# Kernel optimization log

Hardware: AMD Instinct MI355X
Metric: run time of the kernel (lower is better)

The kernel has to match this reference:

```python
import jax, jax.numpy as jnp
import numpy as np

B, L, D, T = 32, 1024, 1024, 10  # batch, seq_len, d_model, num_tags


def setup_inputs() -> dict:
    key = jax.random.key(0)
    ks = jax.random.split(key, 6)
    embeddings = jax.random.normal(ks[0], (B, L, D), jnp.float32)
    attention_mask = jnp.ones((B, L), jnp.int32)  # torchcrf requires mask[:,0]==1
    labels = jax.random.randint(ks[1], (B, L), 0, T)
    conv_w = jax.random.normal(ks[2], (T, D, 3), jnp.float32) * 0.02  # [out,in,k] torch layout
    conv_b = jnp.zeros((T,), jnp.float32)
    start_transitions = jax.random.uniform(ks[3], (T,), jnp.float32, -0.1, 0.1)
    end_transitions = jax.random.uniform(ks[4], (T,), jnp.float32, -0.1, 0.1)
    transitions = jax.random.uniform(ks[5], (T, T), jnp.float32, -0.1, 0.1)
    return dict(embeddings=embeddings, attention_mask=attention_mask, labels=labels,
                conv_w=conv_w, conv_b=conv_b, start_transitions=start_transitions,
                end_transitions=end_transitions, transitions=transitions)


def _crf_nll(emissions, labels, mask_bool, start_transitions, end_transitions, transitions):
    # emissions [B,L,T], labels [B,L] int, mask_bool [B,L]
    b, l, t = emissions.shape
    maskf = mask_bool.astype(emissions.dtype)
    # ---- numerator: score of the given tag path ----
    em_tag = jnp.take_along_axis(emissions, labels[..., None], axis=-1)[..., 0]  # [B,L]
    trans_sc = transitions[labels[:, :-1], labels[:, 1:]]                         # [B,L-1]
    num = start_transitions[labels[:, 0]] + em_tag[:, 0]
    num = num + ((trans_sc + em_tag[:, 1:]) * maskf[:, 1:]).sum(-1)
    seq_len = maskf.sum(-1).astype(jnp.int32)                                     # [B]
    last_tags = labels[jnp.arange(b), seq_len - 1]
    num = num + end_transitions[last_tags]
    # ---- denominator: forward algorithm (log partition), lax.scan over time ----
    alpha0 = start_transitions + emissions[:, 0]                                  # [B,T]

    def step(alpha, xs):
        em_t, m_t = xs  # [B,T], [B]
        nxt = jax.nn.logsumexp(alpha[:, :, None] + transitions[None] + em_t[:, None, :], axis=1)
        return jnp.where(m_t[:, None], nxt, alpha), None

    alpha, _ = jax.lax.scan(step, alpha0,
                            (emissions[:, 1:].transpose(1, 0, 2), mask_bool[:, 1:].T))
    denom = jax.nn.logsumexp(alpha + end_transitions, axis=1)                     # [B]
    return -(num - denom).sum()  # torchcrf reduction='sum', model negates


def reference(embeddings, attention_mask, labels, conv_w, conv_b,
              start_transitions, end_transitions, transitions):
    # Conv1d(d_model -> num_tags, k=3, padding='same') on [B,D,L]
    x = embeddings.transpose(0, 2, 1)  # [B,D,L]
    em = jax.lax.conv_general_dilated(x, conv_w, (1,), 'SAME',
                                      dimension_numbers=('NCH', 'OIH', 'NCH'))
    em = em.transpose(0, 2, 1) + conv_b  # [B,L,T]
    mask_bool = attention_mask.astype(bool)
    return _crf_nll(em, labels, mask_bool, start_transitions, end_transitions, transitions)
```

## Files before the change

### kernel.cpp

```cpp
#include <hip/hip_runtime.h>


#define LNEG -1e30f

static constexpr int B = 32, L = 1024, D = 1024;
static constexpr int CS = 64;
static constexpr int NC = 16;

static constexpr size_t EMPAD_OFF    = 0;
static constexpr size_t CHUNKP_OFF   = (size_t)B * L * 16;
static constexpr size_t CHUNKOFF_OFF = CHUNKP_OFF + (size_t)B * NC * 100;
static constexpr size_t WB_OFF       = CHUNKOFF_OFF + (size_t)B * NC * 12;

typedef __attribute__((ext_vector_type(8))) short short8;
typedef __attribute__((ext_vector_type(4))) short short4v;
typedef __attribute__((ext_vector_type(4))) float v4f;

static __device__ inline short f2bf(float f) {
    unsigned u = __float_as_uint(f);
    unsigned r = (u + 0x7FFFu + ((u >> 16) & 1u)) >> 16;
    return (short)r;
}

__global__ __launch_bounds__(256) void init_kernel(
    const float* __restrict__ w, short* __restrict__ WB, float* __restrict__ out)
{
    const int gid    = blockIdx.x * 256 + threadIdx.x;
    const int stride = gridDim.x * 256;
    for (int i = gid; i < 49152; i += stride) {
        const int k8 = i >> 7;
        const int r  = i & 127;
        const int t  = r >> 3;
        const int j  = r & 7;
        const int k  = (k8 << 3) | j;
        const int kk = k >> 10;
        const int d  = k & 1023;
        WB[i] = (t < 10) ? f2bf(w[t * (D * 3) + d * 3 + kk]) : (short)0;
    }
    if (gid == 0) out[0] = 0.f;
}

static constexpr int SROW = 136;
static constexpr int LDSN = 18 * SROW;

__global__ __launch_bounds__(64) void conv_mfma_kernel(
    const float* __restrict__ emb, const short* __restrict__ WB,
    const float* __restrict__ bias, float* __restrict__ emPad)
{
    __shared__ short lds[2 * LDSN];

    const int lane = threadIdx.x;
    const int b    = blockIdx.x >> 6;
    const int l0   = (blockIdx.x & 63) << 4;
    const int g    = lane >> 4;
    const int m    = lane & 15;

    const float* embB = emb + (size_t)b * (L * D);

    v4f acc0 = {0.f, 0.f, 0.f, 0.f};
    v4f acc1 = {0.f, 0.f, 0.f, 0.f};
    v4f acc2 = {0.f, 0.f, 0.f, 0.f};

    float4 pre[9];

#define PREF(CH) do {                                                         \
    const int d0_ = (CH) * 128;                                               \
    _Pragma("unroll")                                                         \
    for (int it = 0; it < 9; ++it) {                                          \
        const int idx = lane + it * 64;                                       \
        const int r_ = idx >> 5, c4 = idx & 31;                               \
        const int gl = l0 + r_ - 1;                                           \
        float4 v = make_float4(0.f, 0.f, 0.f, 0.f);                           \
        if ((unsigned)gl < (unsigned)L)                                       \
            v = *(const float4*)(embB + (size_t)gl * D + d0_ + c4 * 4);       \
        pre[it] = v;                                                          \
    } } while (0)

#define COMMIT(BUF) do {                                                      \
    short* base_ = lds + (BUF) * LDSN;                                        \
    _Pragma("unroll")                                                         \
    for (int it = 0; it < 9; ++it) {                                          \
        const int idx = lane + it * 64;                                       \
        const int r_ = idx >> 5, c4 = idx & 31;                               \
        short4v s;                                                            \
        s.x = f2bf(pre[it].x); s.y = f2bf(pre[it].y);                         \
        s.z = f2bf(pre[it].z); s.w = f2bf(pre[it].w);                         \
        *(short4v*)(base_ + r_ * SROW + c4 * 4) = s;                          \
    } } while (0)

    PREF(0);
    COMMIT(0);
    __syncthreads();

    for (int dc = 0; dc < 8; ++dc) {
        if (dc < 7) PREF(dc + 1);

        const short* bufp = lds + (dc & 1) * LDSN;
#pragma unroll
        for (int kk = 0; kk < 3; ++kk) {
            const short* arow = bufp + (m + kk) * SROW + g * 8;
            const short* wp   = WB + ((size_t)(kk * 128 + dc * 16 + g)) * 128 + m * 8;
#pragma unroll
            for (int ds = 0; ds < 4; ++ds) {
                const short8 a  = *(const short8*)(arow + ds * 32);
                const short8 bf = *(const short8*)(wp + (size_t)ds * 4 * 128);
                if (kk == 0)      acc0 = __builtin_amdgcn_mfma_f32_16x16x32_bf16(a, bf, acc0, 0, 0, 0);
                else if (kk == 1) acc1 = __builtin_amdgcn_mfma_f32_16x16x32_bf16(a, bf, acc1, 0, 0, 0);
                else              acc2 = __builtin_amdgcn_mfma_f32_16x16x32_bf16(a, bf, acc2, 0, 0, 0);
            }
        }

        if (dc < 7) COMMIT((dc + 1) & 1);
        __syncthreads();
    }
#undef PREF
#undef COMMIT

    const float bt = (m < 10) ? bias[m] : 0.f;
#pragma unroll
    for (int r = 0; r < 4; ++r) {
        const int row = g * 4 + r;
        const int pos = l0 + row;
        const float v = (m < 10) ? (acc0[r] + acc1[r] + acc2[r] + bt) : LNEG;
        emPad[((size_t)(b * L + pos) << 4) + m] = v;
    }
}

__global__ __launch_bounds__(64) void crf_chunk_kernel(
    const float* __restrict__ emPad, const float* __restrict__ trans,
    const float* __restrict__ startT, const float* __restrict__ endT,
    const int* __restrict__ labels,
    float* __restrict__ chunkP, float* __restrict__ chunkOff,
    float* __restrict__ out)
{
    const int lane = threadIdx.x & 63;
    const int grp  = lane >> 4;
    const int i    = lane & 15;
    const int id   = blockIdx.x * 4 + grp;
    const int b    = id >> 4;
    const int c    = id & 15;

    float E[10][10];
#pragma unroll
    for (int k = 0; k < 10; ++k)
#pragma unroll
        for (int j = 0; j < 10; ++j)
            E[k][j] = __expf(trans[k * 10 + j]);

    float P[10];
#pragma unroll
    for (int j = 0; j < 10; ++j) P[j] = (i == j) ? 1.f : 0.f;
    float off = 0.f;

    const int l0 = 1 + c * CS;
    const int n  = min(CS, L - l0);
    const float* embp = emPad + ((size_t)(b * L + l0) << 4);

    float4 nx0 = *(const float4*)(embp);
    float4 nx1 = *(const float4*)(embp + 4);
    float2 nx2 = *(const float2*)(embp + 8);

    for (int s = 0; s < n; ++s) {
        const float4 e0 = nx0;
        const float4 e1 = nx1;
        const float2 e2 = nx2;
        if (s + 1 < n) {
            const float* p = embp + ((size_t)(s + 1) << 4);
            nx0 = *(const float4*)(p);
            nx1 = *(const float4*)(p + 4);
            nx2 = *(const float2*)(p + 8);
        }
        float sj[10];
        sj[0] = __expf(e0.x); sj[1] = __expf(e0.y); sj[2] = __expf(e0.z); sj[3] = __expf(e0.w);
        sj[4] = __expf(e1.x); sj[5] = __expf(e1.y); sj[6] = __expf(e1.z); sj[7] = __expf(e1.w);
        sj[8] = __expf(e2.x); sj[9] = __expf(e2.y);

        float C[10];
#pragma unroll
        for (int j = 0; j < 10; ++j) C[j] = P[0] * E[0][j];
#pragma unroll
        for (int k = 1; k < 10; ++k)
#pragma unroll
            for (int j = 0; j < 10; ++j)
                C[j] = fmaf(P[k], E[k][j], C[j]);
#pragma unroll
        for (int j = 0; j < 10; ++j) C[j] *= sj[j];

        float r = C[0];
#pragma unroll
        for (int j = 1; j < 10; ++j) r = fmaxf(r, C[j]);
        r = fmaxf(r, 1e-30f);
        const float inv = 1.f / r;
        off += __logf(r);
#pragma unroll
        for (int j = 0; j < 10; ++j) P[j] = C[j] * inv;
    }

    if (i < 10) {
        float* op = chunkP + (size_t)id * 100 + i * 10;
#pragma unroll
        for (int j = 0; j < 10; ++j) op[j] = P[j];
        chunkOff[id * 12 + i] = off;
    }

    const int* lab = labels + b * L;
    float part = 0.f;
#pragma unroll
    for (int q = 0; q < 4; ++q) {
        const int o = q * 16 + i;
        if (o < n) {
            const int pos = l0 + o;
            const int y  = lab[pos];
            const int yp = lab[pos - 1];
            part += emPad[((size_t)(b * L + pos) << 4) + y] + trans[yp * 10 + y];
            if (pos == L - 1) part += endT[y];
        }
    }
    if (c == 0 && i == 0) {
        const int y0 = lab[0];
        part += startT[y0] + emPad[((size_t)(b * L) << 4) + y0];
    }
#pragma unroll
    for (int sft = 8; sft >= 1; sft >>= 1) part += __shfl_xor(part, sft);
    if (i == 0) atomicAdd(out, -part);
}

__global__ __launch_bounds__(64) void crf_final_kernel(
    const float* __restrict__ emPad, const float* __restrict__ chunkP,
    const float* __restrict__ chunkOff, const float* __restrict__ startT,
    const float* __restrict__ endT, float* __restrict__ out)
{
    const int b = threadIdx.x;
    if (b >= B) return;

    float PA[10];
    float offA;
    {
        const float* e0 = emPad + ((size_t)(b * L) << 4);
        float A[10];
#pragma unroll
        for (int j = 0; j < 10; ++j) A[j] = startT[j] + e0[j];
        float m0 = A[0];
#pragma unroll
        for (int j = 1; j < 10; ++j) m0 = fmaxf(m0, A[j]);
#pragma unroll
        for (int j = 0; j < 10; ++j) PA[j] = __expf(A[j] - m0);
        offA = m0;
    }

    for (int c = 0; c < NC; ++c) {
        const int id = b * NC + c;
        const float* mp = chunkP + (size_t)id * 100;
        const float* op = chunkOff + id * 12;

        float mat[100];
#pragma unroll
        for (int q = 0; q < 25; ++q)
            *(float4*)&mat[q * 4] = *(const float4*)(mp + q * 4);
        float off[10];
#pragma unroll
        for (int k = 0; k < 10; ++k) off[k] = op[k];

        float mB = off[0];
#pragma unroll
        for (int k = 1; k < 10; ++k) mB = fmaxf(mB, off[k]);
        float gk[10];
#pragma unroll
        for (int k = 0; k < 10; ++k) gk[k] = PA[k] * __expf(off[k] - mB);

        float C[10];
#pragma unroll
        for (int j = 0; j < 10; ++j) C[j] = gk[0] * mat[j];
#pragma unroll
        for (int k = 1; k < 10; ++k)
#pragma unroll
            for (int j = 0; j < 10; ++j)
                C[j] = fmaf(gk[k], mat[k * 10 + j], C[j]);

        float r = C[0];
#pragma unroll
        for (int j = 1; j < 10; ++j) r = fmaxf(r, C[j]);
        r = fmaxf(r, 1e-30f);
        const float inv = 1.f / r;
        offA += mB + __logf(r);
#pragma unroll
        for (int j = 0; j < 10; ++j) PA[j] = C[j] * inv;
    }

    float s = 0.f;
#pragma unroll
    for (int j = 0; j < 10; ++j) s += PA[j] * __expf(endT[j]);
    atomicAdd(out, offA + __logf(s));
}

extern "C" void kernel_launch(void* const* d_in, const int* in_sizes, int n_in,
                              void* d_out, int out_size, void* d_ws, size_t ws_size,
                              hipStream_t stream)
{
    const float* emb    = (const float*)d_in[0];
    const int*   labels = (const int*)d_in[2];
    const float* conv_w = (const float*)d_in[3];
    const float* conv_b = (const float*)d_in[4];
    const float* startT = (const float*)d_in[5];
    const float* endT   = (const float*)d_in[6];
    const float* trans  = (const float*)d_in[7];

    float* ws       = (float*)d_ws;
    float* emPad    = ws + EMPAD_OFF;
    float* chunkP   = ws + CHUNKP_OFF;
    float* chunkOff = ws + CHUNKOFF_OFF;
    short* WB       = (short*)(ws + WB_OFF);
    float* outp     = (float*)d_out;

    hipLaunchKernelGGL(init_kernel, dim3(64), dim3(256), 0, stream,
                       conv_w, WB, outp);
    hipLaunchKernelGGL(conv_mfma_kernel, dim3(B * 64), dim3(64), 0, stream,
                       emb, WB, conv_b, emPad);
    hipLaunchKernelGGL(crf_chunk_kernel, dim3(B * NC / 4), dim3(64), 0, stream,
                       emPad, trans, startT, endT, labels, chunkP, chunkOff, outp);
    hipLaunchKernelGGL(crf_final_kernel, dim3(1), dim3(64), 0, stream,
                       emPad, chunkP, chunkOff, startT, endT, outp);
}
```

Baseline: 272.4 us.

## Split conv reduction over D into two halves combined with atomics

The conv kernel now splits the D reduction across two blocks per (batch, 16-row tile), doubling the grid to 4096 single-wave blocks. Partial sums are combined with atomicAdd into emPad. The init kernel pre-fills emPad with bias and the padding value, and its grid grows to 256 blocks. The intent is more parallelism and latency hiding for the memory-bound conv, at the cost of an extra full-size emPad write pass, atomic traffic, and non-deterministic summation order.

```diff
diff --git a/kernel.cpp b/kernel.cpp
--- a/kernel.cpp
+++ b/kernel.cpp
@@ -23,10 +23,16 @@
 }
 
 __global__ __launch_bounds__(256) void init_kernel(
-    const float* __restrict__ w, short* __restrict__ WB, float* __restrict__ out)
+    const float* __restrict__ w, const float* __restrict__ bias,
+    float* __restrict__ emPad, short* __restrict__ WB, float* __restrict__ out)
 {
     const int gid    = blockIdx.x * 256 + threadIdx.x;
     const int stride = gridDim.x * 256;
+
+    for (int i = gid; i < B * L * 16; i += stride) {
+        const int t = i & 15;
+        emPad[i] = (t < 10) ? bias[t] : LNEG;
+    }
     for (int i = gid; i < 49152; i += stride) {
         const int k8 = i >> 7;
         const int r  = i & 127;
@@ -45,13 +51,15 @@
 
 __global__ __launch_bounds__(64) void conv_mfma_kernel(
     const float* __restrict__ emb, const short* __restrict__ WB,
-    const float* __restrict__ bias, float* __restrict__ emPad)
+    float* __restrict__ emPad)
 {
     __shared__ short lds[2 * LDSN];
 
     const int lane = threadIdx.x;
-    const int b    = blockIdx.x >> 6;
-    const int l0   = (blockIdx.x & 63) << 4;
+    const unsigned bid = blockIdx.x;
+    const int dh   = bid & 1;
+    const int l0   = ((bid >> 1) & 63) << 4;
+    const int b    = bid >> 7;
     const int g    = lane >> 4;
     const int m    = lane & 15;
 
@@ -63,8 +71,8 @@
 
     float4 pre[9];
 
-#define PREF(CH) do {                                                         \
-    const int d0_ = (CH) * 128;                                               \
+#define PREF(DC) do {                                                         \
+    const int d0_ = (DC) * 128;                                               \
     _Pragma("unroll")                                                         \
     for (int it = 0; it < 9; ++it) {                                          \
         const int idx = lane + it * 64;                                       \
@@ -88,14 +96,16 @@
         *(short4v*)(base_ + r_ * SROW + c4 * 4) = s;                          \
     } } while (0)
 
-    PREF(0);
+    const int dcBase = dh * 4;
+    PREF(dcBase);
     COMMIT(0);
     __syncthreads();
 
-    for (int dc = 0; dc < 8; ++dc) {
-        if (dc < 7) PREF(dc + 1);
-
-        const short* bufp = lds + (dc & 1) * LDSN;
+    for (int q = 0; q < 4; ++q) {
+        const int dc = dcBase + q;
+        if (q < 3) PREF(dc + 1);
+
+        const short* bufp = lds + (q & 1) * LDSN;
 #pragma unroll
         for (int kk = 0; kk < 3; ++kk) {
             const short* arow = bufp + (m + kk) * SROW + g * 8;
@@ -110,19 +120,20 @@
             }
         }
 
-        if (dc < 7) COMMIT((dc + 1) & 1);
+        if (q < 3) COMMIT((q + 1) & 1);
         __syncthreads();
     }
 #undef PREF
 #undef COMMIT
 
-    const float bt = (m < 10) ? bias[m] : 0.f;
-#pragma unroll
-    for (int r = 0; r < 4; ++r) {
-        const int row = g * 4 + r;
-        const int pos = l0 + row;
-        const float v = (m < 10) ? (acc0[r] + acc1[r] + acc2[r] + bt) : LNEG;
-        emPad[((size_t)(b * L + pos) << 4) + m] = v;
+    if (m < 10) {
+#pragma unroll
+        for (int r = 0; r < 4; ++r) {
+            const int row = g * 4 + r;
+            const int pos = l0 + row;
+            atomicAdd(&emPad[((size_t)(b * L + pos) << 4) + m],
+                      acc0[r] + acc1[r] + acc2[r]);
+        }
     }
 }
 
@@ -312,10 +323,10 @@
     short* WB       = (short*)(ws + WB_OFF);
     float* outp     = (float*)d_out;
 
-    hipLaunchKernelGGL(init_kernel, dim3(64), dim3(256), 0, stream,
-                       conv_w, WB, outp);
-    hipLaunchKernelGGL(conv_mfma_kernel, dim3(B * 64), dim3(64), 0, stream,
-                       emb, WB, conv_b, emPad);
+    hipLaunchKernelGGL(init_kernel, dim3(256), dim3(256), 0, stream,
+                       conv_w, conv_b, emPad, WB, outp);
+    hipLaunchKernelGGL(conv_mfma_kernel, dim3(B * 64 * 2), dim3(64), 0, stream,
+                       emb, WB, emPad);
     hipLaunchKernelGGL(crf_chunk_kernel, dim3(B * NC / 4), dim3(64), 0, stream,
                        emPad, trans, startT, endT, labels, chunkP, chunkOff, outp);
     hipLaunchKernelGGL(crf_final_kernel, dim3(1), dim3(64), 0, stream,
```

Result: faster. 262.0 us (-3.8%).
